# Kernel tuning notes

Hardware: AMD Instinct MI355X
Metric: run time of the kernel (lower is better)

The kernel has to match this reference:

```python
import jax, jax.numpy as jnp
import numpy as np


def setup_inputs() -> dict:
    key = jax.random.key(0)
    ks = jax.random.split(key, 8)
    B, N, D, E = 8, 64, 64, 32
    nodes = jax.random.normal(ks[0], (B, N, D), dtype=jnp.float32)
    edges = jax.random.normal(ks[1], (B, N * N, E), dtype=jnp.float32)
    mask = jax.random.uniform(ks[2], (B, N * N, 1), dtype=jnp.float32)
    W_e = jax.random.normal(ks[3], (E, D * D), dtype=jnp.float32) * 0.05
    b_e = jnp.zeros((D * D,), dtype=jnp.float32)
    gru_kernel = jax.random.normal(ks[4], (D, 3 * D), dtype=jnp.float32) * 0.05
    gru_rkernel = jax.random.normal(ks[5], (D, 3 * D), dtype=jnp.float32) * 0.05
    gru_bias = jnp.zeros((2, 3 * D), dtype=jnp.float32)
    return {"nodes": nodes, "edges": edges, "mask": mask, "W_e": W_e,
            "b_e": b_e, "gru_kernel": gru_kernel, "gru_rkernel": gru_rkernel,
            "gru_bias": gru_bias}


def _gru_step(x, h, K, R, bias):
    # keras GRU with reset_after=True
    D = h.shape[-1]
    xk = x @ K + bias[0]          # [M, 3D]
    hk = h @ R + bias[1]          # [M, 3D]
    xz, xr, xh = xk[:, :D], xk[:, D:2 * D], xk[:, 2 * D:]
    hz, hr, hh_ = hk[:, :D], hk[:, D:2 * D], hk[:, 2 * D:]
    z = jax.nn.sigmoid(xz + hz)
    r = jax.nn.sigmoid(xr + hr)
    hh = jnp.tanh(xh + r * hh_)
    return z * h + (1.0 - z) * hh


def reference(nodes, edges, mask, W_e, b_e, gru_kernel, gru_rkernel, gru_bias):
    B, N, D = nodes.shape
    # edge-conditioned transform matrices: [B, N*N, D, D]
    A = jax.nn.relu(edges @ W_e + b_e).reshape(B, N * N, D, D)
    # state_j = tile(nodes, [1, N, 1]) -> [B, N*N, D]
    state_j = jnp.tile(nodes, (1, N, 1))
    # per-edge small matmul A @ node_j
    messages = jnp.einsum('beij,bej->bei', A, state_j)  # [B, N*N, D]
    masked = (messages * mask).reshape(B, N, N, D)
    agg = masked.sum(axis=2)  # [B, N, D]
    # GRU over length-2 sequence [old_state, agg_messages], batch B*N, h0=0
    h = jnp.zeros((B * N, D), dtype=nodes.dtype)
    h = _gru_step(nodes.reshape(B * N, D), h, gru_kernel, gru_rkernel, gru_bias)
    h = _gru_step(agg.reshape(B * N, D), h, gru_kernel, gru_rkernel, gru_bias)
    return h.reshape(B, N, D)
```

## Files before the change

### kernel.cpp

```cpp
#include <hip/hip_runtime.h>

typedef _Float16 half8 __attribute__((ext_vector_type(8)));
typedef _Float16 half4 __attribute__((ext_vector_type(4)));
typedef float floatx4 __attribute__((ext_vector_type(4)));

#define BB 8
#define NN 64
#define DD 64
#define EE 32

__global__ void prep_kernel(const float* __restrict__ W_e,
                            const float* __restrict__ edges,
                            _Float16* __restrict__ WT,
                            _Float16* __restrict__ Eh) {
    int blk = blockIdx.x;
    if (blk < 16) {
        int d = blk * 256 + threadIdx.x;
        half8 buf[4];
#pragma unroll
        for (int k = 0; k < 32; ++k) {
            float v = W_e[k * 4096 + d];
            buf[k >> 3][k & 7] = (_Float16)v;
        }
#pragma unroll
        for (int q = 0; q < 4; ++q)
            *reinterpret_cast<half8*>(WT + d * 32 + q * 8) = buf[q];
    } else {
        int idx = ((blk - 16) * 256 + threadIdx.x) * 4;
        floatx4 v = *reinterpret_cast<const floatx4*>(edges + idx);
        half4 h;
        h[0] = (_Float16)v[0]; h[1] = (_Float16)v[1];
        h[2] = (_Float16)v[2]; h[3] = (_Float16)v[3];
        *reinterpret_cast<half4*>(Eh + idx) = h;
    }
}

__global__ __launch_bounds__(256, 2)
void mp_kernel(const _Float16* __restrict__ WT,
               const _Float16* __restrict__ Eh,
               const float* __restrict__ nodes,
               const float* __restrict__ mask,
               const float* __restrict__ b_e,
               float* __restrict__ agg) {
    const int b     = blockIdx.x >> 6;
    const int inode = blockIdx.x & 63;
    const int tid   = threadIdx.x;
    const int w     = tid >> 6;
    const int lane  = tid & 63;
    const int quad  = lane >> 4;
    const int col   = lane & 15;

    __shared__ float S[4][64][33];
    __shared__ float P[4][64];

    half8 ef[4];
#pragma unroll
    for (int eb = 0; eb < 4; ++eb) {
        int ge = b * 4096 + inode * 64 + eb * 16 + col;
        ef[eb] = *reinterpret_cast<const half8*>(Eh + ge * 32 + quad * 8);
    }

    float xm[4][4];
#pragma unroll
    for (int eb = 0; eb < 4; ++eb) {
        int j = eb * 16 + col;
        float mk = mask[b * 4096 + inode * 64 + j];
#pragma unroll
        for (int r = 0; r < 4; ++r) {
            int jj = w * 16 + quad * 4 + r;
            xm[eb][r] = mk * nodes[(b * 64 + j) * 64 + jj];
        }
    }

    const _Float16* aptr = WT + (w * 16 + col) * 32 + quad * 8;
    const float*    bptr = b_e + w * 16 + quad * 4;

    half8  af = *reinterpret_cast<const half8*>(aptr);
    floatx4 bf = *reinterpret_cast<const floatx4*>(bptr);

    for (int i = 0; i < 64; ++i) {
        int inx = (i + 1) & 63;
        half8  af_n = *reinterpret_cast<const half8*>(aptr + inx * 64 * 32);
        floatx4 bf_n = *reinterpret_cast<const floatx4*>(bptr + inx * 64);

        floatx4 c0 = __builtin_amdgcn_mfma_f32_16x16x32_f16(af, ef[0], bf, 0, 0, 0);
        floatx4 c1 = __builtin_amdgcn_mfma_f32_16x16x32_f16(af, ef[1], bf, 0, 0, 0);
        floatx4 c2 = __builtin_amdgcn_mfma_f32_16x16x32_f16(af, ef[2], bf, 0, 0, 0);
        floatx4 c3 = __builtin_amdgcn_mfma_f32_16x16x32_f16(af, ef[3], bf, 0, 0, 0);

        float s = 0.f;
#pragma unroll
        for (int r = 0; r < 4; ++r) {
            s += fmaxf(c0[r], 0.f) * xm[0][r];
            s += fmaxf(c1[r], 0.f) * xm[1][r];
            s += fmaxf(c2[r], 0.f) * xm[2][r];
            s += fmaxf(c3[r], 0.f) * xm[3][r];
        }
        s += __shfl_xor(s, 32);
        if (lane < 32) S[w][i][lane] = s;

        af = af_n; bf = bf_n;
    }
    __syncthreads();

    {
        int i = tid & 63, ww = tid >> 6;
        float p = 0.f;
#pragma unroll
        for (int l = 0; l < 32; ++l) p += S[ww][i][l];
        P[ww][i] = p;
    }
    __syncthreads();
    if (tid < 64)
        agg[(b * 64 + inode) * 64 + tid] = P[0][tid] + P[1][tid] + P[2][tid] + P[3][tid];
}

__device__ __forceinline__ float sigmoidf_(float x) {
    return 1.f / (1.f + __expf(-x));
}
__device__ __forceinline__ float tanhf_(float x) {
    float e = __expf(2.f * x);
    return (e - 1.f) / (e + 1.f);
}

__global__ void gru_kernel(const float* __restrict__ nodes,
                           const float* __restrict__ agg,
                           const float* __restrict__ K,
                           const float* __restrict__ R,
                           const float* __restrict__ bias,
                           float* __restrict__ out) {
    const int row = blockIdx.x;
    const int d   = threadIdx.x;
    __shared__ float xs[64], h1s[64], x2s[64];
    xs[d]  = nodes[row * 64 + d];
    x2s[d] = agg[row * 64 + d];
    __syncthreads();

    float xz = bias[d], xr = bias[64 + d], xh = bias[128 + d];
    for (int k = 0; k < 64; ++k) {
        float xv = xs[k];
        xz = fmaf(xv, K[k * 192 + d], xz);
        xr = fmaf(xv, K[k * 192 + 64 + d], xr);
        xh = fmaf(xv, K[k * 192 + 128 + d], xh);
    }
    float hz = bias[192 + d], hr = bias[256 + d], hh0 = bias[320 + d];
    float z = sigmoidf_(xz + hz);
    float r = sigmoidf_(xr + hr);
    float hh = tanhf_(xh + r * hh0);
    float h = (1.f - z) * hh;
    h1s[d] = h;
    __syncthreads();

    xz = bias[d]; xr = bias[64 + d]; xh = bias[128 + d];
    hz = bias[192 + d]; hr = bias[256 + d]; hh0 = bias[320 + d];
    for (int k = 0; k < 64; ++k) {
        float xv = x2s[k], hv = h1s[k];
        xz = fmaf(xv, K[k * 192 + d], xz);
        xr = fmaf(xv, K[k * 192 + 64 + d], xr);
        xh = fmaf(xv, K[k * 192 + 128 + d], xh);
        hz = fmaf(hv, R[k * 192 + d], hz);
        hr = fmaf(hv, R[k * 192 + 64 + d], hr);
        hh0 = fmaf(hv, R[k * 192 + 128 + d], hh0);
    }
    float z2 = sigmoidf_(xz + hz);
    float r2 = sigmoidf_(xr + hr);
    float hh2 = tanhf_(xh + r2 * hh0);
    out[row * 64 + d] = z2 * h + (1.f - z2) * hh2;
}

extern "C" void kernel_launch(void* const* d_in, const int* in_sizes, int n_in,
                              void* d_out, int out_size, void* d_ws, size_t ws_size,
                              hipStream_t stream) {
    const float* nodes = (const float*)d_in[0];
    const float* edges = (const float*)d_in[1];
    const float* mask  = (const float*)d_in[2];
    const float* W_e   = (const float*)d_in[3];
    const float* b_e   = (const float*)d_in[4];
    const float* gk    = (const float*)d_in[5];
    const float* gr    = (const float*)d_in[6];
    const float* gb    = (const float*)d_in[7];
    float* out = (float*)d_out;

    char* ws = (char*)d_ws;
    _Float16* WT = (_Float16*)ws;
    _Float16* Eh = (_Float16*)(ws + 262144);
    float*    agg = (float*)(ws + 262144 + 2097152);

    prep_kernel<<<1040, 256, 0, stream>>>(W_e, edges, WT, Eh);
    mp_kernel<<<512, 256, 0, stream>>>(WT, Eh, nodes, mask, b_e, agg);
    gru_kernel<<<512, 64, 0, stream>>>(nodes, agg, gk, gr, gb, out);
}
```

Before: 104.2 us.

## Fuse edge conversion and GRU into message-passing kernel, drop intermediate buffers

Result: faster. 99.96 us (-4.1%).

```diff
diff --git a/kernel.cpp b/kernel.cpp
--- a/kernel.cpp
+++ b/kernel.cpp
@@ -1,47 +1,45 @@
 #include <hip/hip_runtime.h>
 
 typedef _Float16 half8 __attribute__((ext_vector_type(8)));
-typedef _Float16 half4 __attribute__((ext_vector_type(4)));
 typedef float floatx4 __attribute__((ext_vector_type(4)));
+typedef float floatx2 __attribute__((ext_vector_type(2)));
 
 #define BB 8
 #define NN 64
 #define DD 64
 #define EE 32
 
-__global__ void prep_kernel(const float* __restrict__ W_e,
-                            const float* __restrict__ edges,
-                            _Float16* __restrict__ WT,
-                            _Float16* __restrict__ Eh) {
-    int blk = blockIdx.x;
-    if (blk < 16) {
-        int d = blk * 256 + threadIdx.x;
-        half8 buf[4];
+__global__ void prep_w_kernel(const float* __restrict__ W_e,
+                              _Float16* __restrict__ WT) {
+    const int d  = blockIdx.x * 64 + (threadIdx.x & 63);
+    const int kq = threadIdx.x >> 6;
+    half8 buf;
 #pragma unroll
-        for (int k = 0; k < 32; ++k) {
-            float v = W_e[k * 4096 + d];
-            buf[k >> 3][k & 7] = (_Float16)v;
-        }
-#pragma unroll
-        for (int q = 0; q < 4; ++q)
-            *reinterpret_cast<half8*>(WT + d * 32 + q * 8) = buf[q];
-    } else {
-        int idx = ((blk - 16) * 256 + threadIdx.x) * 4;
-        floatx4 v = *reinterpret_cast<const floatx4*>(edges + idx);
-        half4 h;
-        h[0] = (_Float16)v[0]; h[1] = (_Float16)v[1];
-        h[2] = (_Float16)v[2]; h[3] = (_Float16)v[3];
-        *reinterpret_cast<half4*>(Eh + idx) = h;
-    }
+    for (int j = 0; j < 8; ++j)
+        buf[j] = (_Float16)W_e[(kq * 8 + j) * 4096 + d];
+    *reinterpret_cast<half8*>(WT + d * 32 + kq * 8) = buf;
+}
+
+__device__ __forceinline__ floatx2 relu2(floatx2 v) {
+    floatx2 z = {0.f, 0.f};
+    return __builtin_elementwise_max(v, z);
+}
+__device__ __forceinline__ float sigmoidf_(float x) { return 1.f / (1.f + __expf(-x)); }
+__device__ __forceinline__ float tanhf_(float x) {
+    float e = __expf(2.f * x);
+    return (e - 1.f) / (e + 1.f);
 }
 
 __global__ __launch_bounds__(256, 2)
-void mp_kernel(const _Float16* __restrict__ WT,
-               const _Float16* __restrict__ Eh,
-               const float* __restrict__ nodes,
-               const float* __restrict__ mask,
-               const float* __restrict__ b_e,
-               float* __restrict__ agg) {
+void fused_kernel(const _Float16* __restrict__ WT,
+                  const float* __restrict__ edges,
+                  const float* __restrict__ nodes,
+                  const float* __restrict__ mask,
+                  const float* __restrict__ b_e,
+                  const float* __restrict__ K,
+                  const float* __restrict__ R,
+                  const float* __restrict__ bias,
+                  float* __restrict__ out) {
     const int b     = blockIdx.x >> 6;
     const int inode = blockIdx.x & 63;
     const int tid   = threadIdx.x;
@@ -49,18 +47,29 @@
     const int lane  = tid & 63;
     const int quad  = lane >> 4;
     const int col   = lane & 15;
+    const int row   = b * 64 + inode;
 
-    __shared__ float S[4][64][33];
+    __shared__ float S[4][64][17];
     __shared__ float P[4][64];
+    __shared__ float xs[64], aggs[64], h1s[64];
+    __shared__ float g1[192], g2[192];
+
+    if (tid < 64) xs[tid] = nodes[row * 64 + tid];
 
     half8 ef[4];
 #pragma unroll
     for (int eb = 0; eb < 4; ++eb) {
-        int ge = b * 4096 + inode * 64 + eb * 16 + col;
-        ef[eb] = *reinterpret_cast<const half8*>(Eh + ge * 32 + quad * 8);
+        const float* ep = edges + (b * 4096 + inode * 64 + eb * 16 + col) * 32 + quad * 8;
+        floatx4 e0 = *reinterpret_cast<const floatx4*>(ep);
+        floatx4 e1 = *reinterpret_cast<const floatx4*>(ep + 4);
+#pragma unroll
+        for (int j = 0; j < 4; ++j) {
+            ef[eb][j]     = (_Float16)e0[j];
+            ef[eb][4 + j] = (_Float16)e1[j];
+        }
     }
 
-    float xm[4][4];
+    floatx2 xm[4][2];
 #pragma unroll
     for (int eb = 0; eb < 4; ++eb) {
         int j = eb * 16 + col;
@@ -68,104 +77,85 @@
 #pragma unroll
         for (int r = 0; r < 4; ++r) {
             int jj = w * 16 + quad * 4 + r;
-            xm[eb][r] = mk * nodes[(b * 64 + j) * 64 + jj];
+            xm[eb][r >> 1][r & 1] = mk * nodes[(b * 64 + j) * 64 + jj];
         }
     }
 
     const _Float16* aptr = WT + (w * 16 + col) * 32 + quad * 8;
     const float*    bptr = b_e + w * 16 + quad * 4;
 
-    half8  af = *reinterpret_cast<const half8*>(aptr);
+    half8   af = *reinterpret_cast<const half8*>(aptr);
     floatx4 bf = *reinterpret_cast<const floatx4*>(bptr);
 
     for (int i = 0; i < 64; ++i) {
         int inx = (i + 1) & 63;
-        half8  af_n = *reinterpret_cast<const half8*>(aptr + inx * 64 * 32);
+        half8   af_n = *reinterpret_cast<const half8*>(aptr + inx * 64 * 32);
         floatx4 bf_n = *reinterpret_cast<const floatx4*>(bptr + inx * 64);
 
-        floatx4 c0 = __builtin_amdgcn_mfma_f32_16x16x32_f16(af, ef[0], bf, 0, 0, 0);
-        floatx4 c1 = __builtin_amdgcn_mfma_f32_16x16x32_f16(af, ef[1], bf, 0, 0, 0);
-        floatx4 c2 = __builtin_amdgcn_mfma_f32_16x16x32_f16(af, ef[2], bf, 0, 0, 0);
-        floatx4 c3 = __builtin_amdgcn_mfma_f32_16x16x32_f16(af, ef[3], bf, 0, 0, 0);
+        floatx4 c[4];
+        c[0] = __builtin_amdgcn_mfma_f32_16x16x32_f16(af, ef[0], bf, 0, 0, 0);
+        c[1] = __builtin_amdgcn_mfma_f32_16x16x32_f16(af, ef[1], bf, 0, 0, 0);
+        c[2] = __builtin_amdgcn_mfma_f32_16x16x32_f16(af, ef[2], bf, 0, 0, 0);
+        c[3] = __builtin_amdgcn_mfma_f32_16x16x32_f16(af, ef[3], bf, 0, 0, 0);
 
-        float s = 0.f;
+        floatx2 sv = {0.f, 0.f};
 #pragma unroll
-        for (int r = 0; r < 4; ++r) {
-            s += fmaxf(c0[r], 0.f) * xm[0][r];
-            s += fmaxf(c1[r], 0.f) * xm[1][r];
-            s += fmaxf(c2[r], 0.f) * xm[2][r];
-            s += fmaxf(c3[r], 0.f) * xm[3][r];
+        for (int eb = 0; eb < 4; ++eb) {
+            floatx2* cp = reinterpret_cast<floatx2*>(&c[eb]);
+            sv += relu2(cp[0]) * xm[eb][0];
+            sv += relu2(cp[1]) * xm[eb][1];
         }
+        float s = sv[0] + sv[1];
         s += __shfl_xor(s, 32);
-        if (lane < 32) S[w][i][lane] = s;
+        s += __shfl_xor(s, 16);
+        if (lane < 16) S[w][i][lane] = s;
 
         af = af_n; bf = bf_n;
     }
     __syncthreads();
 
     {
-        int i = tid & 63, ww = tid >> 6;
+        int ii = tid & 63, ww = tid >> 6;
         float p = 0.f;
 #pragma unroll
-        for (int l = 0; l < 32; ++l) p += S[ww][i][l];
-        P[ww][i] = p;
+        for (int l = 0; l < 16; ++l) p += S[ww][ii][l];
+        P[ww][ii] = p;
     }
     __syncthreads();
-    if (tid < 64)
-        agg[(b * 64 + inode) * 64 + tid] = P[0][tid] + P[1][tid] + P[2][tid] + P[3][tid];
-}
-
-__device__ __forceinline__ float sigmoidf_(float x) {
-    return 1.f / (1.f + __expf(-x));
-}
-__device__ __forceinline__ float tanhf_(float x) {
-    float e = __expf(2.f * x);
-    return (e - 1.f) / (e + 1.f);
-}
-
-__global__ void gru_kernel(const float* __restrict__ nodes,
-                           const float* __restrict__ agg,
-                           const float* __restrict__ K,
-                           const float* __restrict__ R,
-                           const float* __restrict__ bias,
-                           float* __restrict__ out) {
-    const int row = blockIdx.x;
-    const int d   = threadIdx.x;
-    __shared__ float xs[64], h1s[64], x2s[64];
-    xs[d]  = nodes[row * 64 + d];
-    x2s[d] = agg[row * 64 + d];
+    if (tid < 64) aggs[tid] = P[0][tid] + P[1][tid] + P[2][tid] + P[3][tid];
     __syncthreads();
 
-    float xz = bias[d], xr = bias[64 + d], xh = bias[128 + d];
-    for (int k = 0; k < 64; ++k) {
-        float xv = xs[k];
-        xz = fmaf(xv, K[k * 192 + d], xz);
-        xr = fmaf(xv, K[k * 192 + 64 + d], xr);
-        xh = fmaf(xv, K[k * 192 + 128 + d], xh);
+    if (tid < 192) {
+        float acc = bias[tid];
+#pragma unroll 4
+        for (int k = 0; k < 64; ++k) acc = fmaf(xs[k], K[k * 192 + tid], acc);
+        g1[tid] = acc;
     }
-    float hz = bias[192 + d], hr = bias[256 + d], hh0 = bias[320 + d];
-    float z = sigmoidf_(xz + hz);
-    float r = sigmoidf_(xr + hr);
-    float hh = tanhf_(xh + r * hh0);
-    float h = (1.f - z) * hh;
-    h1s[d] = h;
+    __syncthreads();
+    if (tid < 64) {
+        float z  = sigmoidf_(g1[tid]       + bias[192 + tid]);
+        float r  = sigmoidf_(g1[64 + tid]  + bias[256 + tid]);
+        float hh = tanhf_  (g1[128 + tid] + r * bias[320 + tid]);
+        h1s[tid] = (1.f - z) * hh;
+    }
     __syncthreads();
 
-    xz = bias[d]; xr = bias[64 + d]; xh = bias[128 + d];
-    hz = bias[192 + d]; hr = bias[256 + d]; hh0 = bias[320 + d];
-    for (int k = 0; k < 64; ++k) {
-        float xv = x2s[k], hv = h1s[k];
-        xz = fmaf(xv, K[k * 192 + d], xz);
-        xr = fmaf(xv, K[k * 192 + 64 + d], xr);
-        xh = fmaf(xv, K[k * 192 + 128 + d], xh);
-        hz = fmaf(hv, R[k * 192 + d], hz);
-        hr = fmaf(hv, R[k * 192 + 64 + d], hr);
-        hh0 = fmaf(hv, R[k * 192 + 128 + d], hh0);
+    if (tid < 192) {
+        float a1 = bias[tid], a2 = bias[192 + tid];
+#pragma unroll 4
+        for (int k = 0; k < 64; ++k) {
+            a1 = fmaf(aggs[k], K[k * 192 + tid], a1);
+            a2 = fmaf(h1s[k],  R[k * 192 + tid], a2);
+        }
+        g1[tid] = a1; g2[tid] = a2;
     }
-    float z2 = sigmoidf_(xz + hz);
-    float r2 = sigmoidf_(xr + hr);
-    float hh2 = tanhf_(xh + r2 * hh0);
-    out[row * 64 + d] = z2 * h + (1.f - z2) * hh2;
+    __syncthreads();
+    if (tid < 64) {
+        float z  = sigmoidf_(g1[tid]       + g2[tid]);
+        float r  = sigmoidf_(g1[64 + tid]  + g2[64 + tid]);
+        float hh = tanhf_  (g1[128 + tid] + r * g2[128 + tid]);
+        out[row * 64 + tid] = z * h1s[tid] + (1.f - z) * hh;
+    }
 }
 
 extern "C" void kernel_launch(void* const* d_in, const int* in_sizes, int n_in,
@@ -181,12 +171,8 @@
     const float* gb    = (const float*)d_in[7];
     float* out = (float*)d_out;
 
-    char* ws = (char*)d_ws;
-    _Float16* WT = (_Float16*)ws;
-    _Float16* Eh = (_Float16*)(ws + 262144);
-    float*    agg = (float*)(ws + 262144 + 2097152);
+    _Float16* WT = (_Float16*)d_ws;
 
-    prep_kernel<<<1040, 256, 0, stream>>>(W_e, edges, WT, Eh);
-    mp_kernel<<<512, 256, 0, stream>>>(WT, Eh, nodes, mask, b_e, agg);
-    gru_kernel<<<512, 64, 0, stream>>>(nodes, agg, gk, gr, gb, out);
+    prep_w_kernel<<<64, 256, 0, stream>>>(W_e, WT);
+    fused_kernel<<<512, 256, 0, stream>>>(WT, edges, nodes, mask, b_e, gk, gr, gb, out);
 }
```
